# Kernel tuning notes

Hardware: AMD Instinct MI355X
Metric: run time of the kernel (lower is better)

Reference implementation:

```python
import jax, jax.numpy as jnp
import numpy as np

D = 32          # max_delay_block
NEG_INF = -1e13 # matches module's self.neg_inf


def setup_inputs() -> dict:
    key = jax.random.key(0)
    ks = jax.random.split(key, 8)
    b, c, t, f, h = 2, 128, 512, 64, 32
    xm = jax.random.normal(ks[0], (b, c, t, f), dtype=jnp.float32)
    xf = jax.random.normal(ks[1], (b, c, t, f), dtype=jnp.float32)
    # pointwise_conv1 / pointwise_conv2: 1x1 convs == per-pixel linear maps c->h
    w1 = jax.random.normal(ks[2], (c, h), dtype=jnp.float32) * (1.0 / np.sqrt(c))
    b1 = jax.random.normal(ks[3], (h,), dtype=jnp.float32) * 0.01
    w2 = jax.random.normal(ks[4], (c, h), dtype=jnp.float32) * (1.0 / np.sqrt(c))
    b2 = jax.random.normal(ks[5], (h,), dtype=jnp.float32) * 0.01
    # conv2d: h -> 1 channels, kernel (5,3)   (OIHW layout)
    wc = jax.random.normal(ks[6], (1, h, 5, 3), dtype=jnp.float32) * (1.0 / np.sqrt(h * 15))
    bc = jax.random.normal(ks[7], (1,), dtype=jnp.float32) * 0.01
    return {"xm": xm, "xf": xf, "w1": w1, "b1": b1, "w2": w2, "b2": b2, "wc": wc, "bc": bc}


def reference(xm, xf, w1, b1, w2, b2, wc, bc):
    b, c, t, f = xf.shape
    # 1x1 convs (per time-freq bin linear projections)
    xm1 = jnp.einsum('bctf,ch->bhtf', xm, w1) + b1[None, :, None, None]
    xf1 = jnp.einsum('bctf,ch->bhtf', xf, w2) + b2[None, :, None, None]

    # delay windows: window j at frame i looks at original frame i + j - (D-1)
    # (j = D-1 is zero delay, j = 0 is delay D-1; out-of-range frames are zero-padded)
    idx = jnp.arange(t)[:, None] + jnp.arange(D)[None, :]          # [t, D] into padded time
    xf1p = jnp.pad(xf1, ((0, 0), (0, 0), (D - 1, 0), (0, 0)))      # [b,h,t+D-1,f]
    win = xf1p[:, :, idx, :]                                       # [b,h,t,D,f]
    corr = jnp.einsum('bhtf,bhtdf->bhtd', xm1, win)                # [b,h,t,D]

    # conv2d smoothing: kernel (5,3), pad (3,1) -> height t+2, keep first t rows
    corr1 = jax.lax.conv_general_dilated(
        corr, wc, window_strides=(1, 1), padding=((3, 3), (1, 1)),
        dimension_numbers=('NCHW', 'OIHW', 'NCHW'))
    corr1 = corr1[:, 0, :t, :] + bc[0]                             # [b,t,D]

    # causal mask: frame i cannot attend to delays pointing before frame 0,
    # i.e. positions with i + j < D - 1 get neg_inf (exactly tril().flip() logic)
    bad = (jnp.arange(t)[:, None] + jnp.arange(D)[None, :]) < (D - 1)
    corr1 = jnp.where(bad[None, :, :], NEG_INF, corr1)
    w = jax.nn.softmax(corr1, axis=-1)                             # [b,t,D]

    # delay-weighted sum over the raw far-end features
    xfp = jnp.pad(xf, ((0, 0), (0, 0), (D - 1, 0), (0, 0)))        # [b,c,t+D-1,f]
    win2 = xfp[:, :, idx, :]                                       # [b,c,t,D,f]
    out = jnp.einsum('btd,bctdf->bctf', w, win2)                   # [b,c,t,f]
    return out
```

## Files before the change

### kernel.cpp

```cpp
#include <hip/hip_runtime.h>

typedef unsigned short u16;
typedef unsigned int   u32;

#define B_ 2
#define C_ 128
#define T_ 512
#define F_ 64
#define H_ 32
#define D_ 32

#define XM1_OUT 0u
#define XF1_OUT 2097152u

#define CORR_OFF 0u
#define WQ_OFF   1127168u

__global__ __launch_bounds__(256) void k1_proj(const float* __restrict__ xm, const float* __restrict__ xf,
                                               const float* __restrict__ w1, const float* __restrict__ b1,
                                               const float* __restrict__ w2, const float* __restrict__ b2,
                                               float* __restrict__ xm1, float* __restrict__ xf1){
  int blk  = blockIdx.x;
  int mblk = blk & 127;
  int bt   = blk >> 7;
  int b    = bt >> 1, sel = bt & 1;
  int m0   = mblk * 256;
  int tid  = threadIdx.x;

  const float* X    = (sel ? xf : xm) + (size_t)b * (C_*T_*F_) + m0;
  const float* W    = sel ? w2 : w1;
  const float* bias = sel ? b2 : b1;

  __shared__ float wls[C_*H_];
#pragma unroll
  for (int i = 0; i < 4; i++)
    *(float4*)(wls + i*1024 + tid*4) = *(const float4*)(W + i*1024 + tid*4);

  int mg = tid & 63;
  int hg = tid >> 6;
  const float* Xm = X + (mg << 2);

  float4 acc[8];
#pragma unroll
  for (int j = 0; j < 8; j++) acc[j] = make_float4(0.f,0.f,0.f,0.f);

  float4 buf[8];
#pragma unroll
  for (int i = 0; i < 8; i++)
    buf[i] = *(const float4*)(Xm + (size_t)i * (T_*F_));

  __syncthreads();

#define FMA4(A, Wv) do { \
    A.x = fmaf((Wv), xv.x, A.x); A.y = fmaf((Wv), xv.y, A.y); \
    A.z = fmaf((Wv), xv.z, A.z); A.w = fmaf((Wv), xv.w, A.w); } while (0)

#define K1_BODY(c_) do {                                                  \
    const float* wk = wls + (c_)*H_ + hg*8;                               \
    float4 wa = *(const float4*)(wk);                                     \
    float4 wb = *(const float4*)(wk + 4);                                 \
    FMA4(acc[0], wa.x); FMA4(acc[1], wa.y); FMA4(acc[2], wa.z); FMA4(acc[3], wa.w); \
    FMA4(acc[4], wb.x); FMA4(acc[5], wb.y); FMA4(acc[6], wb.z); FMA4(acc[7], wb.w); \
  } while (0)

  for (int cb = 0; cb < 15; cb++){
#pragma unroll
    for (int i = 0; i < 8; i++){
      float4 xv = buf[i];
      buf[i] = *(const float4*)(Xm + (size_t)(cb*8 + 8 + i) * (T_*F_));
      K1_BODY(cb*8 + i);
    }
  }
#pragma unroll
  for (int i = 0; i < 8; i++){
    float4 xv = buf[i];
    K1_BODY(120 + i);
  }

  float* O = (sel ? xf1 : xm1) + (size_t)b * (H_*T_*F_) + m0 + (mg << 2);
#pragma unroll
  for (int j = 0; j < 8; j++){
    int h = hg*8 + j;
    float bv = bias[h];
    float4 o = make_float4(acc[j].x + bv, acc[j].y + bv, acc[j].z + bv, acc[j].w + bv);
    *(float4*)(O + (size_t)h * (T_*F_)) = o;
  }
#undef FMA4
#undef K1_BODY
}

#define BSW(r) ((((r) >> 3) & 7) << 2)

__global__ __launch_bounds__(256) void k2_corr(const float* __restrict__ xm1, const float* __restrict__ xf1,
                                               float* __restrict__ corr_pad){
  int blk = blockIdx.x;
  int tt = blk & 7, h = (blk >> 3) & 31, b = blk >> 8;
  int t0 = tt * 64;
  const float* A  = xm1 + ((size_t)(b*H_ + h)) * (T_*F_);
  const float* Bm = xf1 + ((size_t)(b*H_ + h)) * (T_*F_);

  __shared__ float Al[64*68];
  __shared__ float Bl[95*68];
  int tid = threadIdx.x;

  for (int idx = tid; idx < 64*16; idx += 256){
    int r = idx >> 4, q = idx & 15;
    *(float4*)(Al + r*68 + q*4) = *(const float4*)(A + (size_t)(t0 + r)*F_ + q*4);
  }
  for (int idx = tid; idx < 95*16; idx += 256){
    int r = idx >> 4, q = idx & 15;
    int gr = t0 - 31 + r;
    float4 v = make_float4(0.f,0.f,0.f,0.f);
    if (gr >= 0) v = *(const float4*)(Bm + (size_t)gr*F_ + q*4);
    *(float4*)(Bl + r*68 + ((q*4) ^ BSW(r))) = v;
  }
  __syncthreads();

  int tl = tid >> 2, dg = tid & 3;
  float acc[8];
#pragma unroll
  for (int j = 0; j < 8; j++) acc[j] = 0.f;

  for (int fq = 0; fq < 16; fq++){
    float4 a = *(const float4*)(Al + tl*68 + fq*4);
#pragma unroll
    for (int j = 0; j < 8; j++){
      int rbj = tl + dg*8 + j;
      float4 bv = *(const float4*)(Bl + rbj*68 + ((fq*4) ^ BSW(rbj)));
      acc[j] += a.x*bv.x + a.y*bv.y + a.z*bv.z + a.w*bv.w;
    }
  }
  float* o = corr_pad + ((size_t)(b*H_ + h))*(518*34) + (size_t)(t0 + tl + 3)*34 + (dg*8 + 1);
#pragma unroll
  for (int j = 0; j < 8; j++) o[j] = acc[j];
}

__global__ __launch_bounds__(256) void k3_conv_softmax(const float* __restrict__ corr_pad,
                                                       const float* __restrict__ wc, const float* __restrict__ bc,
                                                       float* __restrict__ wq){
  int b  = blockIdx.x >> 6;
  int t0 = (blockIdx.x & 63) * 8;
  int tid = threadIdx.x;

  __shared__ float ls[32*12*34];
  const float* cp = corr_pad + (size_t)b * (H_*518*34);
  for (int idx = tid; idx < 32*12*34; idx += 256){
    int h = idx / 408, rem = idx - h*408;
    int r = rem / 34, dd = rem - r*34;
    int gr = t0 + r;
    bool halo = (gr < 3) | (gr > 514) | (dd == 0) | (dd == 33);
    ls[idx] = halo ? 0.f : cp[(size_t)h*(518*34) + (size_t)gr*34 + dd];
  }
  __syncthreads();

  int tl = tid >> 5, d = tid & 31;
  int t = t0 + tl;

  float val = bc[0];
  for (int h = 0; h < H_; h++){
    const float* base = ls + h*408 + tl*34 + d;
    const float* wch = wc + h*15;
#pragma unroll
    for (int kh = 0; kh < 5; kh++){
#pragma unroll
      for (int kw = 0; kw < 3; kw++){
        val += base[kh*34 + kw] * wch[kh*3 + kw];
      }
    }
  }
  if (t + d < D_ - 1) val = -1e13f;

  float m = val;
#pragma unroll
  for (int off = 16; off > 0; off >>= 1) m = fmaxf(m, __shfl_xor(m, off));
  float e = __expf(val - m);
  float s = e;
#pragma unroll
  for (int off = 16; off > 0; off >>= 1) s += __shfl_xor(s, off);

  wq[((size_t)b*T_ + t)*D_ + d] = e / s;
}

__global__ __launch_bounds__(256) void k4_out(const float* __restrict__ xf, const float* __restrict__ wq,
                                              float* __restrict__ out){
  int blk = blockIdx.x;
  int tt = blk & 7, c = (blk >> 3) & 127, b = blk >> 10;
  int t0 = tt * 64;
  const float* Xf = xf + ((size_t)(b*C_ + c)) * (T_*F_);

  __shared__ float xfl[95*68];
  __shared__ float wl[64*33];
  int tid = threadIdx.x;

  for (int idx = tid; idx < 95*16; idx += 256){
    int r = idx >> 4, q = idx & 15;
    int gr = t0 - 31 + r;
    float4 v = make_float4(0.f,0.f,0.f,0.f);
    if (gr >= 0) v = *(const float4*)(Xf + (size_t)gr*F_ + q*4);
    *(float4*)(xfl + r*68 + q*4) = v;
  }
  for (int idx = tid; idx < 64*8; idx += 256){
    int r = idx >> 3, q = idx & 7;
    float4 v = *(const float4*)(wq + ((size_t)b*T_ + t0 + r)*D_ + q*4);
    wl[r*33 + q*4 + 0] = v.x; wl[r*33 + q*4 + 1] = v.y;
    wl[r*33 + q*4 + 2] = v.z; wl[r*33 + q*4 + 3] = v.w;
  }
  __syncthreads();

  int tg = tid >> 4, q = tid & 15;
  float4 acc[4];
#pragma unroll
  for (int j = 0; j < 4; j++) acc[j] = make_float4(0.f,0.f,0.f,0.f);

#pragma unroll
  for (int rr = 0; rr < 35; rr++){
    float4 xv = *(const float4*)(xfl + (tg*4 + rr)*68 + q*4);
#pragma unroll
    for (int j = 0; j < 4; j++){
      int d = rr - j;
      if (d >= 0 && d < D_){
        float wv = wl[(tg*4 + j)*33 + d];
        acc[j].x += wv * xv.x; acc[j].y += wv * xv.y;
        acc[j].z += wv * xv.z; acc[j].w += wv * xv.w;
      }
    }
  }
#pragma unroll
  for (int j = 0; j < 4; j++){
    int t = t0 + tg*4 + j;
    float* O = out + (((size_t)(b*C_ + c))*T_ + t)*F_ + q*4;
    *(float4*)O = acc[j];
  }
}

extern "C" void kernel_launch(void* const* d_in, const int* in_sizes, int n_in,
                              void* d_out, int out_size, void* d_ws, size_t ws_size,
                              hipStream_t stream) {
  const float* xm = (const float*)d_in[0];
  const float* xf = (const float*)d_in[1];
  const float* w1 = (const float*)d_in[2];
  const float* b1 = (const float*)d_in[3];
  const float* w2 = (const float*)d_in[4];
  const float* b2 = (const float*)d_in[5];
  const float* wc = (const float*)d_in[6];
  const float* bc = (const float*)d_in[7];
  float* ws = (float*)d_ws;

  float* xm1 = (float*)d_out + XM1_OUT;
  float* xf1 = (float*)d_out + XF1_OUT;

  hipLaunchKernelGGL(k1_proj, dim3(512), dim3(256), 0, stream, xm, xf, w1, b1, w2, b2, xm1, xf1);
  hipLaunchKernelGGL(k2_corr, dim3(512), dim3(256), 0, stream, xm1, xf1, ws + CORR_OFF);
  hipLaunchKernelGGL(k3_conv_softmax, dim3(128), dim3(256), 0, stream, ws + CORR_OFF, wc, bc, ws + WQ_OFF);
  hipLaunchKernelGGL(k4_out, dim3(2048), dim3(256), 0, stream, xf, ws + WQ_OFF, (float*)d_out);
}
```

Measured before the change: 172.5 us.

## Split projection channel reduction across four thread groups with shared-memory reduce

```diff
diff --git a/kernel.cpp b/kernel.cpp
--- a/kernel.cpp
+++ b/kernel.cpp
@@ -16,37 +16,39 @@
 #define CORR_OFF 0u
 #define WQ_OFF   1127168u
 
-__global__ __launch_bounds__(256) void k1_proj(const float* __restrict__ xm, const float* __restrict__ xf,
-                                               const float* __restrict__ w1, const float* __restrict__ b1,
-                                               const float* __restrict__ w2, const float* __restrict__ b2,
-                                               float* __restrict__ xm1, float* __restrict__ xf1){
+__global__ __launch_bounds__(1024, 4) void k1_proj(const float* __restrict__ xm, const float* __restrict__ xf,
+                                                   const float* __restrict__ w1, const float* __restrict__ b1,
+                                                   const float* __restrict__ w2, const float* __restrict__ b2,
+                                                   float* __restrict__ xm1, float* __restrict__ xf1){
   int blk  = blockIdx.x;
   int mblk = blk & 127;
   int bt   = blk >> 7;
   int b    = bt >> 1, sel = bt & 1;
   int m0   = mblk * 256;
   int tid  = threadIdx.x;
+  int g    = tid >> 8;
+  int s    = tid & 255;
+  int mg   = s & 63;
+  int hg   = s >> 6;
 
   const float* X    = (sel ? xf : xm) + (size_t)b * (C_*T_*F_) + m0;
   const float* W    = sel ? w2 : w1;
   const float* bias = sel ? b2 : b1;
 
   __shared__ float wls[C_*H_];
+  __shared__ float red[2][256][36];
+
+  *(float4*)(wls + tid*4) = *(const float4*)(W + tid*4);
+
+  const float* Xm = X + (size_t)(32*g) * (T_*F_) + (mg << 2);
+
+  float4 acc[8];
+#pragma unroll
+  for (int j = 0; j < 8; j++) acc[j] = make_float4(0.f,0.f,0.f,0.f);
+
+  float4 buf[4];
 #pragma unroll
   for (int i = 0; i < 4; i++)
-    *(float4*)(wls + i*1024 + tid*4) = *(const float4*)(W + i*1024 + tid*4);
-
-  int mg = tid & 63;
-  int hg = tid >> 6;
-  const float* Xm = X + (mg << 2);
-
-  float4 acc[8];
-#pragma unroll
-  for (int j = 0; j < 8; j++) acc[j] = make_float4(0.f,0.f,0.f,0.f);
-
-  float4 buf[8];
-#pragma unroll
-  for (int i = 0; i < 8; i++)
     buf[i] = *(const float4*)(Xm + (size_t)i * (T_*F_));
 
   __syncthreads();
@@ -55,38 +57,56 @@
     A.x = fmaf((Wv), xv.x, A.x); A.y = fmaf((Wv), xv.y, A.y); \
     A.z = fmaf((Wv), xv.z, A.z); A.w = fmaf((Wv), xv.w, A.w); } while (0)
 
-#define K1_BODY(c_) do {                                                  \
-    const float* wk = wls + (c_)*H_ + hg*8;                               \
-    float4 wa = *(const float4*)(wk);                                     \
-    float4 wb = *(const float4*)(wk + 4);                                 \
-    FMA4(acc[0], wa.x); FMA4(acc[1], wa.y); FMA4(acc[2], wa.z); FMA4(acc[3], wa.w); \
-    FMA4(acc[4], wb.x); FMA4(acc[5], wb.y); FMA4(acc[6], wb.z); FMA4(acc[7], wb.w); \
-  } while (0)
-
-  for (int cb = 0; cb < 15; cb++){
-#pragma unroll
-    for (int i = 0; i < 8; i++){
-      float4 xv = buf[i];
-      buf[i] = *(const float4*)(Xm + (size_t)(cb*8 + 8 + i) * (T_*F_));
-      K1_BODY(cb*8 + i);
-    }
-  }
-#pragma unroll
-  for (int i = 0; i < 8; i++){
-    float4 xv = buf[i];
-    K1_BODY(120 + i);
-  }
-
-  float* O = (sel ? xf1 : xm1) + (size_t)b * (H_*T_*F_) + m0 + (mg << 2);
-#pragma unroll
-  for (int j = 0; j < 8; j++){
-    int h = hg*8 + j;
-    float bv = bias[h];
-    float4 o = make_float4(acc[j].x + bv, acc[j].y + bv, acc[j].z + bv, acc[j].w + bv);
-    *(float4*)(O + (size_t)h * (T_*F_)) = o;
+#pragma unroll
+  for (int k = 0; k < 32; k++){
+    float4 xv = buf[k & 3];
+    if (k < 28)
+      buf[k & 3] = *(const float4*)(Xm + (size_t)(k + 4) * (T_*F_));
+    const float* wk = wls + (32*g + k)*H_ + hg*8;
+    float4 wa = *(const float4*)(wk);
+    float4 wb = *(const float4*)(wk + 4);
+    FMA4(acc[0], wa.x); FMA4(acc[1], wa.y); FMA4(acc[2], wa.z); FMA4(acc[3], wa.w);
+    FMA4(acc[4], wb.x); FMA4(acc[5], wb.y); FMA4(acc[6], wb.z); FMA4(acc[7], wb.w);
   }
 #undef FMA4
-#undef K1_BODY
+
+  if (g >= 2){
+    float* r = &red[g-2][s][0];
+#pragma unroll
+    for (int j = 0; j < 8; j++) *(float4*)(r + j*4) = acc[j];
+  }
+  __syncthreads();
+  if (g < 2){
+    const float* r = &red[g][s][0];
+#pragma unroll
+    for (int j = 0; j < 8; j++){
+      float4 v = *(const float4*)(r + j*4);
+      acc[j].x += v.x; acc[j].y += v.y; acc[j].z += v.z; acc[j].w += v.w;
+    }
+  }
+  __syncthreads();
+  if (g == 1){
+    float* r = &red[0][s][0];
+#pragma unroll
+    for (int j = 0; j < 8; j++) *(float4*)(r + j*4) = acc[j];
+  }
+  __syncthreads();
+  if (g == 0){
+    const float* r = &red[0][s][0];
+#pragma unroll
+    for (int j = 0; j < 8; j++){
+      float4 v = *(const float4*)(r + j*4);
+      acc[j].x += v.x; acc[j].y += v.y; acc[j].z += v.z; acc[j].w += v.w;
+    }
+    float* O = (sel ? xf1 : xm1) + (size_t)b * (H_*T_*F_) + m0 + (mg << 2);
+#pragma unroll
+    for (int j = 0; j < 8; j++){
+      int h = hg*8 + j;
+      float bv = bias[h];
+      float4 o = make_float4(acc[j].x + bv, acc[j].y + bv, acc[j].z + bv, acc[j].w + bv);
+      *(float4*)(O + (size_t)h * (T_*F_)) = o;
+    }
+  }
 }
 
 #define BSW(r) ((((r) >> 3) & 7) << 2)
@@ -249,7 +269,7 @@
   float* xm1 = (float*)d_out + XM1_OUT;
   float* xf1 = (float*)d_out + XF1_OUT;
 
-  hipLaunchKernelGGL(k1_proj, dim3(512), dim3(256), 0, stream, xm, xf, w1, b1, w2, b2, xm1, xf1);
+  hipLaunchKernelGGL(k1_proj, dim3(512), dim3(1024), 0, stream, xm, xf, w1, b1, w2, b2, xm1, xf1);
   hipLaunchKernelGGL(k2_corr, dim3(512), dim3(256), 0, stream, xm1, xf1, ws + CORR_OFF);
   hipLaunchKernelGGL(k3_conv_softmax, dim3(128), dim3(256), 0, stream, ws + CORR_OFF, wc, bc, ws + WQ_OFF);
   hipLaunchKernelGGL(k4_out, dim3(2048), dim3(256), 0, stream, xf, ws + WQ_OFF, (float*)d_out);
```

Measured after the change: 182.8 us. 6.0% more time.
